# Performance work log

Hardware: AMD Instinct MI355X
Metric: run time of the kernel (lower is better)

## Reference

```python
import jax, jax.numpy as jnp
import numpy as np

EPS = 1e-12  # F.normalize eps


def setup_inputs() -> dict:
    key = jax.random.key(0)
    k1, k2, k3 = jax.random.split(key, 3)
    N, C, H, W, K = 64, 512, 28, 28, 64
    x = jax.random.normal(k1, (N, C, H, W), dtype=jnp.float32)
    conv_w = jax.random.normal(k2, (K, C), dtype=jnp.float32)  # 1x1 conv weight squeezed
    centroids = jax.random.uniform(k3, (K, C), dtype=jnp.float32)  # torch.rand init
    return {"x": x, "conv_w": conv_w, "centroids": centroids}


def reference(x, conv_w, centroids):
    N, C, H, W = x.shape
    K = centroids.shape[0]
    xf = x.reshape(N, C, H * W)                                  # (N, C, L)
    # 1x1 conv == matmul over channels, softmax over cluster dim
    logits = jnp.einsum('kc,ncl->nkl', conv_w, xf)               # (N, K, L)
    a = jax.nn.softmax(logits, axis=1)                           # softmax over clusters
    # vlad[n,k,c] = sum_l a[n,k,l] * (x[n,c,l] - cent[k,c])
    #            = (a @ x^T)[n,k,c] - (sum_l a[n,k,l]) * cent[k,c]
    agg = jnp.einsum('nkl,ncl->nkc', a, xf)                      # (N, K, C)
    vlad = agg - a.sum(axis=-1)[..., None] * centroids[None]     # (N, K, C)
    # intra-normalize per cluster (dim=2)
    vlad = vlad / jnp.maximum(jnp.linalg.norm(vlad, axis=2, keepdims=True), EPS)
    v = vlad.reshape(N, K * C)
    # global L2 normalize
    v = v / jnp.maximum(jnp.linalg.norm(v, axis=1, keepdims=True), EPS)
    return v
```

## Files before the change

### kernel.cpp

```cpp
#include <hip/hip_runtime.h>

#define C_ 512
#define L_ 784
#define K_ 64
#define EPS_ 1e-12f

typedef _Float16 half_t;
typedef _Float16 half4 __attribute__((ext_vector_type(4)));
typedef float float4v __attribute__((ext_vector_type(4)));

__global__ __launch_bounds__(1024) void kF(const float* __restrict__ x,
                                           const float* __restrict__ w,
                                           float* __restrict__ aggP,
                                           float* __restrict__ asumP) {
    __shared__ float  sl[16 * 64 * 4];
    __shared__ half_t ah[64 * 20];

    const int t    = threadIdx.x;
    const int n    = blockIdx.y;
    const int bx   = blockIdx.x;
    const int l0   = bx * 192;
    const int NT   = (bx == 3) ? 13 : 12;
    const int wv   = t >> 6;
    const int lane = t & 63;
    const int m16  = lane & 15;
    const int q    = lane >> 4;
    const int kt   = wv & 3;
    const int cs   = wv >> 2;

    const float* xn = x + (size_t)n * (C_ * L_);
    const float* xr = xn + (size_t)(cs * 128 + m16) * L_ + l0 + 4 * q;

    float4v pf[8];
#pragma unroll
    for (int i = 0; i < 8; ++i)
        pf[i] = *(const float4v*)(xr + (size_t)i * 16 * L_);

    half4 wf[8];
#pragma unroll
    for (int i = 0; i < 8; ++i) {
        float4v f = *(const float4v*)(w + (size_t)(kt * 16 + m16) * C_ +
                                      cs * 128 + i * 16 + 4 * q);
        wf[i] = half4{(half_t)f[0], (half_t)f[1], (half_t)f[2], (half_t)f[3]};
    }
    half4 ifr;
#pragma unroll
    for (int j = 0; j < 4; ++j) ifr[j] = (half_t)((4 * q + j == m16) ? 1.0f : 0.0f);

    const float4v z4 = {0.f, 0.f, 0.f, 0.f};
    float4v agc[8];
#pragma unroll
    for (int i = 0; i < 8; ++i) agc[i] = z4;
    float asum_reg = 0.f;

    for (int s = 0; s < NT; ++s) {
        half4 bh[8];
#pragma unroll
        for (int i = 0; i < 8; ++i)
            bh[i] = half4{(half_t)pf[i][0], (half_t)pf[i][1],
                          (half_t)pf[i][2], (half_t)pf[i][3]};
        if (s + 1 < NT) {
            const float* p = xr + (s + 1) * 16;
#pragma unroll
            for (int i = 0; i < 8; ++i)
                pf[i] = *(const float4v*)(p + (size_t)i * 16 * L_);
        }
        float4v lac0 = z4, lac1 = z4;
#pragma unroll
        for (int i = 0; i < 8; ++i) {
            float4v xt = __builtin_amdgcn_mfma_f32_16x16x16f16(bh[i], ifr, z4, 0, 0, 0);
            half4 a4 = {(half_t)xt[0], (half_t)xt[1], (half_t)xt[2], (half_t)xt[3]};
            if (i < 4) lac0 = __builtin_amdgcn_mfma_f32_16x16x16f16(a4, wf[i], lac0, 0, 0, 0);
            else       lac1 = __builtin_amdgcn_mfma_f32_16x16x16f16(a4, wf[i], lac1, 0, 0, 0);
        }
        float4v lac = lac0 + lac1;
#pragma unroll
        for (int r = 0; r < 4; ++r)
            sl[((4 * q + r) * 64 + kt * 16 + m16) * 4 + cs] = lac[r];
        __syncthreads();
        {
            float4v p4 = *(const float4v*)&sl[(wv * 64 + lane) * 4];
            float lg = p4[0] + p4[1] + p4[2] + p4[3];
            float mx = lg;
#pragma unroll
            for (int off = 32; off; off >>= 1) mx = fmaxf(mx, __shfl_xor(mx, off, 64));
            float e = __expf(lg - mx);
            float sm = e;
#pragma unroll
            for (int off = 32; off; off >>= 1) sm += __shfl_xor(sm, off, 64);
            float a = e / sm;
            asum_reg += a;
            ah[lane * 20 + wv] = (half_t)a;
        }
        __syncthreads();
        half4 aA = *(const half4*)&ah[(kt * 16 + m16) * 20 + 4 * q];
#pragma unroll
        for (int i = 0; i < 8; ++i)
            agc[i] = __builtin_amdgcn_mfma_f32_16x16x16f16(aA, bh[i], agc[i], 0, 0, 0);
    }

    sl[wv * 64 + lane] = asum_reg;
    __syncthreads();
    if (t < 64) {
        float s_ = 0.f;
#pragma unroll
        for (int j = 0; j < 16; ++j) s_ += sl[j * 64 + t];
        asumP[((size_t)n * 4 + bx) * 64 + t] = s_;
    }
    float* ap = aggP + (((size_t)n * 4 + bx) * 64) * (size_t)C_;
#pragma unroll
    for (int i = 0; i < 8; ++i)
#pragma unroll
        for (int r = 0; r < 4; ++r)
            ap[(size_t)(kt * 16 + 4 * q + r) * C_ + (cs * 8 + i) * 16 + m16] = agc[i][r];
}

__global__ __launch_bounds__(256) void kC(const float* __restrict__ aggP,
                                          const float* __restrict__ cent,
                                          const float* __restrict__ asumP,
                                          float* __restrict__ out) {
    __shared__ float asumS[4];
    const int t  = threadIdx.x;
    const int n  = blockIdx.y;
    const int k0 = blockIdx.x * 4;
    if (t < 4) {
        float s = 0.f;
        for (int j = 0; j < 4; ++j) s += asumP[((size_t)n * 4 + j) * 64 + k0 + t];
        asumS[t] = s;
    }
    __syncthreads();
    const int wv   = t >> 6;
    const int lane = t & 63;
    const int k    = k0 + wv;
    const float as = asumS[wv];
    const float* a0 = aggP + (((size_t)n * 4 + 0) * 64 + k) * C_;
    const float* a1 = aggP + (((size_t)n * 4 + 1) * 64 + k) * C_;
    const float* a2 = aggP + (((size_t)n * 4 + 2) * 64 + k) * C_;
    const float* a3 = aggP + (((size_t)n * 4 + 3) * 64 + k) * C_;
    const float* cp = cent + (size_t)k * C_;
    float4v v[2];
    float ss = 0.f;
#pragma unroll
    for (int j = 0; j < 2; ++j) {
        const int c = 4 * lane + 256 * j;
        float4v val = *(const float4v*)(a0 + c);
        val = val + *(const float4v*)(a1 + c);
        val = val + *(const float4v*)(a2 + c);
        val = val + *(const float4v*)(a3 + c);
        float4v c4 = *(const float4v*)(cp + c);
#pragma unroll
        for (int e = 0; e < 4; ++e) {
            val[e] -= as * c4[e];
            ss += val[e] * val[e];
        }
        v[j] = val;
    }
#pragma unroll
    for (int off = 32; off; off >>= 1) ss += __shfl_xor(ss, off, 64);
    const float scale = 1.f / (fmaxf(sqrtf(ss), EPS_) * 8.f);
    float* op = out + (size_t)n * (K_ * C_) + (size_t)k * C_;
#pragma unroll
    for (int j = 0; j < 2; ++j) {
        float4v o = v[j];
#pragma unroll
        for (int e = 0; e < 4; ++e) o[e] *= scale;
        *(float4v*)(op + 4 * lane + 256 * j) = o;
    }
}

extern "C" void kernel_launch(void* const* d_in, const int* in_sizes, int n_in,
                              void* d_out, int out_size, void* d_ws, size_t ws_size,
                              hipStream_t stream) {
    (void)in_sizes; (void)n_in; (void)out_size; (void)ws_size;
    const float* x    = (const float*)d_in[0];
    const float* w    = (const float*)d_in[1];
    const float* cent = (const float*)d_in[2];
    float* out = (float*)d_out;

    char* base = (char*)d_ws;
    float* aggP  = (float*)base;
    float* asumP = aggP + (size_t)64 * 4 * 64 * 512;

    kF<<<dim3(4, 64), 1024, 0, stream>>>(x, w, aggP, asumP);
    kC<<<dim3(16, 64), 256, 0, stream>>>(aggP, cent, asumP, out);
}
```

Baseline: 179.3 us.

## Double-buffer LDS and defer aggregation MFMA to drop a barrier per step

Shared logit and softmax buffers are double-buffered, which removes the second __syncthreads in each L-step. The aggregation MFMAs for step s are moved into step s+1 so they overlap with the next step's softmax, and a final epilogue handles the last step. The logit accumulation is split into four independent MFMA chains instead of two to shorten dependency latency, and a sched_barrier is added after the prefetch loads. This adds register pressure from holding the previous step's fp16 x tile at 1024 threads per block, which could cause spills.

```diff
diff --git a/kernel.cpp b/kernel.cpp
--- a/kernel.cpp
+++ b/kernel.cpp
@@ -13,8 +13,8 @@
                                            const float* __restrict__ w,
                                            float* __restrict__ aggP,
                                            float* __restrict__ asumP) {
-    __shared__ float  sl[16 * 64 * 4];
-    __shared__ half_t ah[64 * 20];
+    __shared__ float  sl[2][16 * 64 * 4];
+    __shared__ half_t ah[2][64 * 20];
 
     const int t    = threadIdx.x;
     const int n    = blockIdx.y;
@@ -51,13 +51,14 @@
     float4v agc[8];
 #pragma unroll
     for (int i = 0; i < 8; ++i) agc[i] = z4;
+    half4 bhp[8];
     float asum_reg = 0.f;
 
     for (int s = 0; s < NT; ++s) {
-        half4 bh[8];
+        half4 bn[8];
 #pragma unroll
         for (int i = 0; i < 8; ++i)
-            bh[i] = half4{(half_t)pf[i][0], (half_t)pf[i][1],
+            bn[i] = half4{(half_t)pf[i][0], (half_t)pf[i][1],
                           (half_t)pf[i][2], (half_t)pf[i][3]};
         if (s + 1 < NT) {
             const float* p = xr + (s + 1) * 16;
@@ -65,21 +66,22 @@
             for (int i = 0; i < 8; ++i)
                 pf[i] = *(const float4v*)(p + (size_t)i * 16 * L_);
         }
-        float4v lac0 = z4, lac1 = z4;
+        __builtin_amdgcn_sched_barrier(0);
+        float4v lc[4] = {z4, z4, z4, z4};
 #pragma unroll
         for (int i = 0; i < 8; ++i) {
-            float4v xt = __builtin_amdgcn_mfma_f32_16x16x16f16(bh[i], ifr, z4, 0, 0, 0);
+            float4v xt = __builtin_amdgcn_mfma_f32_16x16x16f16(bn[i], ifr, z4, 0, 0, 0);
             half4 a4 = {(half_t)xt[0], (half_t)xt[1], (half_t)xt[2], (half_t)xt[3]};
-            if (i < 4) lac0 = __builtin_amdgcn_mfma_f32_16x16x16f16(a4, wf[i], lac0, 0, 0, 0);
-            else       lac1 = __builtin_amdgcn_mfma_f32_16x16x16f16(a4, wf[i], lac1, 0, 0, 0);
-        }
-        float4v lac = lac0 + lac1;
+            lc[i & 3] = __builtin_amdgcn_mfma_f32_16x16x16f16(a4, wf[i], lc[i & 3], 0, 0, 0);
+        }
+        float4v lac = (lc[0] + lc[1]) + (lc[2] + lc[3]);
+        float* slb = sl[s & 1];
 #pragma unroll
         for (int r = 0; r < 4; ++r)
-            sl[((4 * q + r) * 64 + kt * 16 + m16) * 4 + cs] = lac[r];
+            slb[((4 * q + r) * 64 + kt * 16 + m16) * 4 + cs] = lac[r];
         __syncthreads();
         {
-            float4v p4 = *(const float4v*)&sl[(wv * 64 + lane) * 4];
+            float4v p4 = *(const float4v*)&slb[(wv * 64 + lane) * 4];
             float lg = p4[0] + p4[1] + p4[2] + p4[3];
             float mx = lg;
 #pragma unroll
@@ -90,21 +92,33 @@
             for (int off = 32; off; off >>= 1) sm += __shfl_xor(sm, off, 64);
             float a = e / sm;
             asum_reg += a;
-            ah[lane * 20 + wv] = (half_t)a;
-        }
-        __syncthreads();
-        half4 aA = *(const half4*)&ah[(kt * 16 + m16) * 20 + 4 * q];
+            ah[s & 1][lane * 20 + wv] = (half_t)a;
+        }
+        if (s > 0) {
+            half4 aA = *(const half4*)&ah[(s - 1) & 1][(kt * 16 + m16) * 20 + 4 * q];
+#pragma unroll
+            for (int i = 0; i < 8; ++i)
+                agc[i] = __builtin_amdgcn_mfma_f32_16x16x16f16(aA, bhp[i], agc[i], 0, 0, 0);
+        }
+#pragma unroll
+        for (int i = 0; i < 8; ++i) bhp[i] = bn[i];
+    }
+
+    __syncthreads();
+    {
+        half4 aA = *(const half4*)&ah[(NT - 1) & 1][(kt * 16 + m16) * 20 + 4 * q];
 #pragma unroll
         for (int i = 0; i < 8; ++i)
-            agc[i] = __builtin_amdgcn_mfma_f32_16x16x16f16(aA, bh[i], agc[i], 0, 0, 0);
-    }
-
-    sl[wv * 64 + lane] = asum_reg;
+            agc[i] = __builtin_amdgcn_mfma_f32_16x16x16f16(aA, bhp[i], agc[i], 0, 0, 0);
+    }
+
+    float* red = sl[0];
+    red[wv * 64 + lane] = asum_reg;
     __syncthreads();
     if (t < 64) {
         float s_ = 0.f;
 #pragma unroll
-        for (int j = 0; j < 16; ++j) s_ += sl[j * 64 + t];
+        for (int j = 0; j < 16; ++j) s_ += red[j * 64 + t];
         asumP[((size_t)n * 4 + bx) * 64 + t] = s_;
     }
     float* ap = aggP + (((size_t)n * 4 + bx) * 64) * (size_t)C_;
```

Measured after the change: 241.6 us. 34.8% more time.

## Stage x tiles through double-buffered LDS to remove redundant global loads

Applied to the files above, without the earlier changes.

Each of the four k-tile waves sharing a channel slice previously loaded the same x tile from global memory on its own. Now each wave loads two distinct 16x16 tiles per step into a double-buffered shared-memory tile, and all waves read their slice from LDS. This cuts global x traffic by a factor of four. The cost is 64KB of extra LDS, LDS reads and conversions on the critical path, and a scheduling barrier. The logits MFMA chain is also split into four independent accumulators to shorten dependency chains.

```diff
diff --git a/kernel.cpp b/kernel.cpp
--- a/kernel.cpp
+++ b/kernel.cpp
@@ -13,6 +13,7 @@
                                            const float* __restrict__ w,
                                            float* __restrict__ aggP,
                                            float* __restrict__ asumP) {
+    __shared__ float  xs[2][32 * 256];
     __shared__ float  sl[16 * 64 * 4];
     __shared__ half_t ah[64 * 20];
 
@@ -29,12 +30,17 @@
     const int cs   = wv >> 2;
 
     const float* xn = x + (size_t)n * (C_ * L_);
-    const float* xr = xn + (size_t)(cs * 128 + m16) * L_ + l0 + 4 * q;
 
-    float4v pf[8];
-#pragma unroll
-    for (int i = 0; i < 8; ++i)
-        pf[i] = *(const float4v*)(xr + (size_t)i * 16 * L_);
+    const int T0 = 2 * wv;
+    const float* src0 = xn + (size_t)((T0 >> 3) * 128 + (T0 & 7) * 16 + m16) * L_ + l0 + 4 * q;
+    const float* src1 = xn + (size_t)(((T0 + 1) >> 3) * 128 + ((T0 + 1) & 7) * 16 + m16) * L_ + l0 + 4 * q;
+
+    {
+        float4v g0 = *(const float4v*)src0;
+        float4v g1 = *(const float4v*)src1;
+        *(float4v*)&xs[0][T0 * 256 + lane * 4]       = g0;
+        *(float4v*)&xs[0][(T0 + 1) * 256 + lane * 4] = g1;
+    }
 
     half4 wf[8];
 #pragma unroll
@@ -53,27 +59,28 @@
     for (int i = 0; i < 8; ++i) agc[i] = z4;
     float asum_reg = 0.f;
 
+    __syncthreads();
+
     for (int s = 0; s < NT; ++s) {
-        half4 bh[8];
-#pragma unroll
-        for (int i = 0; i < 8; ++i)
-            bh[i] = half4{(half_t)pf[i][0], (half_t)pf[i][1],
-                          (half_t)pf[i][2], (half_t)pf[i][3]};
-        if (s + 1 < NT) {
-            const float* p = xr + (s + 1) * 16;
-#pragma unroll
-            for (int i = 0; i < 8; ++i)
-                pf[i] = *(const float4v*)(p + (size_t)i * 16 * L_);
+        float4v g0, g1;
+        const bool pf = (s + 1 < NT);
+        if (pf) {
+            g0 = *(const float4v*)(src0 + 16 * (s + 1));
+            g1 = *(const float4v*)(src1 + 16 * (s + 1));
         }
-        float4v lac0 = z4, lac1 = z4;
+        __builtin_amdgcn_sched_barrier(0);
+        const float* xb = &xs[s & 1][(cs * 8) * 256];
+        half4 bn[8];
+        float4v lc[4] = {z4, z4, z4, z4};
 #pragma unroll
         for (int i = 0; i < 8; ++i) {
-            float4v xt = __builtin_amdgcn_mfma_f32_16x16x16f16(bh[i], ifr, z4, 0, 0, 0);
+            float4v f = *(const float4v*)&xb[i * 256 + lane * 4];
+            bn[i] = half4{(half_t)f[0], (half_t)f[1], (half_t)f[2], (half_t)f[3]};
+            float4v xt = __builtin_amdgcn_mfma_f32_16x16x16f16(bn[i], ifr, z4, 0, 0, 0);
             half4 a4 = {(half_t)xt[0], (half_t)xt[1], (half_t)xt[2], (half_t)xt[3]};
-            if (i < 4) lac0 = __builtin_amdgcn_mfma_f32_16x16x16f16(a4, wf[i], lac0, 0, 0, 0);
-            else       lac1 = __builtin_amdgcn_mfma_f32_16x16x16f16(a4, wf[i], lac1, 0, 0, 0);
+            lc[i & 3] = __builtin_amdgcn_mfma_f32_16x16x16f16(a4, wf[i], lc[i & 3], 0, 0, 0);
         }
-        float4v lac = lac0 + lac1;
+        float4v lac = (lc[0] + lc[1]) + (lc[2] + lc[3]);
 #pragma unroll
         for (int r = 0; r < 4; ++r)
             sl[((4 * q + r) * 64 + kt * 16 + m16) * 4 + cs] = lac[r];
@@ -92,11 +99,15 @@
             asum_reg += a;
             ah[lane * 20 + wv] = (half_t)a;
         }
+        if (pf) {
+            *(float4v*)&xs[(s + 1) & 1][T0 * 256 + lane * 4]       = g0;
+            *(float4v*)&xs[(s + 1) & 1][(T0 + 1) * 256 + lane * 4] = g1;
+        }
         __syncthreads();
         half4 aA = *(const half4*)&ah[(kt * 16 + m16) * 20 + 4 * q];
 #pragma unroll
         for (int i = 0; i < 8; ++i)
-            agc[i] = __builtin_amdgcn_mfma_f32_16x16x16f16(aA, bh[i], agc[i], 0, 0, 0);
+            agc[i] = __builtin_amdgcn_mfma_f32_16x16x16f16(aA, bn[i], agc[i], 0, 0, 0);
     }
 
     sl[wv * 64 + lane] = asum_reg;
```

After: 172.5 us. 3.8% less time.
